# Performance work log

Hardware: AMD Instinct MI355X
Metric: run time of the kernel (lower is better)

Reference implementation:

```python
import jax, jax.numpy as jnp
import numpy as np

DIM = 2048
DIM_HEAD = 64
NUM_HEADS = 32
FFN_INNER = 4 * DIM  # 8192
SCALE = DIM_HEAD ** -0.5
LN_EPS = 1e-5


def setup_inputs() -> dict:
    key = jax.random.key(0)
    k1, k2, k3 = jax.random.split(key, 3)
    B, S = 2, 2048
    in_dim = FFN_INNER * 2 + DIM_HEAD * (NUM_HEADS + 2)  # 18560
    out_in = FFN_INNER + DIM  # 10240
    return {
        "x": jax.random.normal(k1, (B, S, DIM), jnp.float32),
        "W_in": jax.random.normal(k2, (DIM, in_dim), jnp.float32) * (DIM ** -0.5),
        "W_out": jax.random.normal(k3, (out_in, DIM), jnp.float32) * (out_in ** -0.5),
        "ln_gamma": jnp.ones((DIM,), jnp.float32),
        "ln_beta": jnp.zeros((DIM,), jnp.float32),
    }


def _rotary_pos(seq, d, dtype):
    inv_freq = 1.0 / (10000.0 ** (jnp.arange(0, d, 2, dtype=jnp.float32) / d))
    freqs = jnp.arange(seq, dtype=jnp.float32)[:, None] * inv_freq[None, :]  # [s, d/2]
    pos = jnp.concatenate([freqs, freqs], axis=-1)  # [s, d]
    return pos.astype(dtype)


def _rotate_half(t):
    d = t.shape[-1] // 2
    return jnp.concatenate([-t[..., d:], t[..., :d]], axis=-1)


def _apply_rotary(pos, t):
    return t * jnp.cos(pos) + _rotate_half(t) * jnp.sin(pos)


def reference(x, W_in, W_out, ln_gamma, ln_beta):
    B, S, D = x.shape
    # LayerNorm (residual uses the NORMED x, as in the source)
    mu = jnp.mean(x, axis=-1, keepdims=True)
    var = jnp.mean(jnp.square(x - mu), axis=-1, keepdims=True)
    xn = (x - mu) / jnp.sqrt(var + LN_EPS) * ln_gamma + ln_beta

    h = jnp.einsum('bsd,df->bsf', xn, W_in)  # fused input projection
    a = NUM_HEADS * DIM_HEAD  # attn inner dim
    q = h[..., :a]
    k = h[..., a:a + DIM_HEAD]                      # [b, s, d] shared (multi-query)
    v = h[..., a + DIM_HEAD:a + 2 * DIM_HEAD]       # [b, s, d]
    ffn_input = h[..., a + 2 * DIM_HEAD:a + 2 * DIM_HEAD + FFN_INNER]

    q = q.reshape(B, S, NUM_HEADS, DIM_HEAD).transpose(0, 2, 1, 3)  # b h s d

    pos = _rotary_pos(S, DIM_HEAD, x.dtype)
    q = _apply_rotary(pos, q)
    k = _apply_rotary(pos, k)
    q = q * SCALE

    sim = jnp.einsum('bhsd,bjd->bhsj', q, k)  # [b, h, s, s]
    causal = jnp.triu(jnp.ones((S, S), bool), 1)
    neg = jnp.finfo(sim.dtype).max
    sim = jnp.where(causal, -neg, sim)
    sim = sim - jax.lax.stop_gradient(jnp.max(sim, axis=-1, keepdims=True))
    attn = jax.nn.softmax(sim, axis=-1)

    attn_out = jnp.einsum('bhij,bjd->bhid', attn, v)  # b h s d
    attn_out = attn_out.transpose(0, 2, 1, 3).reshape(B, S, a)

    concat = jnp.concatenate([attn_out, ffn_input], axis=-1)  # [b, s, ffn+dim]
    out = jnp.einsum('bsf,fd->bsd', concat, W_out)
    return out + xn
```

## Files before the change

kernel.cpp:

```cpp
#include <hip/hip_runtime.h>
#include <cstdint>

#define NB     2
#define SEQ    2048
#define DIMN   2048
#define NROWS  (NB*SEQ)
#define NHEADS 32
#define DHEAD  64
#define FFN    8192
#define HC     10368
#define WINLD  18560
#define OI     10240

typedef __bf16 bf16_t;
typedef bf16_t bf16x8 __attribute__((ext_vector_type(8)));
typedef bf16_t bf16x4 __attribute__((ext_vector_type(4)));
typedef bf16_t bf16x2 __attribute__((ext_vector_type(2)));
typedef float  f32x4  __attribute__((ext_vector_type(4)));

typedef const uint32_t __attribute__((address_space(1)))* as1p;
typedef uint32_t __attribute__((address_space(3)))* as3p;

__device__ __forceinline__ void load_lds16(const void* g, void* l) {
  __builtin_amdgcn_global_load_lds(
      reinterpret_cast<as1p>(reinterpret_cast<uintptr_t>(g)),
      reinterpret_cast<as3p>(reinterpret_cast<uintptr_t>(l)),
      16, 0, 0);
}

__global__ __launch_bounds__(256) void ln_kernel(const float* __restrict__ x,
                                                 const float* __restrict__ gamma,
                                                 const float* __restrict__ beta,
                                                 bf16_t* __restrict__ xnb)
{
  const int row = blockIdx.x;
  const int t = threadIdx.x;
  const float4* xr = (const float4*)(x + (size_t)row * DIMN);
  float4 v0 = xr[t], v1 = xr[t + 256];
  float s  = v0.x+v0.y+v0.z+v0.w + v1.x+v1.y+v1.z+v1.w;
  float ss = v0.x*v0.x+v0.y*v0.y+v0.z*v0.z+v0.w*v0.w
           + v1.x*v1.x+v1.y*v1.y+v1.z*v1.z+v1.w*v1.w;
#pragma unroll
  for (int off = 32; off; off >>= 1) { s += __shfl_xor(s, off); ss += __shfl_xor(ss, off); }
  __shared__ float red[8];
  const int w = t >> 6;
  if ((t & 63) == 0) { red[w] = s; red[w + 4] = ss; }
  __syncthreads();
  s  = red[0]+red[1]+red[2]+red[3];
  ss = red[4]+red[5]+red[6]+red[7];
  const float mu   = s * (1.f/DIMN);
  const float var  = ss * (1.f/DIMN) - mu*mu;
  const float rstd = rsqrtf(var + 1e-5f);
  const float4* g4 = (const float4*)gamma;
  const float4* b4 = (const float4*)beta;
  float4 ga0 = g4[t], ga1 = g4[t+256], be0 = b4[t], be1 = b4[t+256];
  float4 y0, y1;
  y0.x = (v0.x-mu)*rstd*ga0.x + be0.x;  y0.y = (v0.y-mu)*rstd*ga0.y + be0.y;
  y0.z = (v0.z-mu)*rstd*ga0.z + be0.z;  y0.w = (v0.w-mu)*rstd*ga0.w + be0.w;
  y1.x = (v1.x-mu)*rstd*ga1.x + be1.x;  y1.y = (v1.y-mu)*rstd*ga1.y + be1.y;
  y1.z = (v1.z-mu)*rstd*ga1.z + be1.z;  y1.w = (v1.w-mu)*rstd*ga1.w + be1.w;
  bf16_t* xo = xnb + (size_t)row * DIMN;
  bf16x4 o0 = {(bf16_t)y0.x, (bf16_t)y0.y, (bf16_t)y0.z, (bf16_t)y0.w};
  bf16x4 o1 = {(bf16_t)y1.x, (bf16_t)y1.y, (bf16_t)y1.z, (bf16_t)y1.w};
  *(bf16x4*)(xo + t*4)        = o0;
  *(bf16x4*)(xo + (t+256)*4)  = o1;
}

__global__ __launch_bounds__(256) void tcast_kernel(const float* __restrict__ in, int ld_in,
                                                    bf16_t* __restrict__ out, int out_cols)
{
  __shared__ float tile[128][33];
  const int t = threadIdx.x;
  const int ic0 = blockIdx.x * 32;
  const int ir0 = blockIdx.y * 128;
#pragma unroll
  for (int k = 0; k < 16; k++) {
    const int idx = k*256 + t, row = idx >> 5, col = idx & 31;
    tile[row][col] = in[(size_t)(ir0 + row) * ld_in + ic0 + col];
  }
  __syncthreads();
#pragma unroll
  for (int k = 0; k < 8; k++) {
    const int idx = k*256 + t, r = idx >> 6, cp = idx & 63;
    bf16x2 v = {(bf16_t)tile[cp*2][r], (bf16_t)tile[cp*2 + 1][r]};
    *(bf16x2*)&out[(size_t)(ic0 + r) * out_cols + ir0 + cp*2] = v;
  }
}

#define BW_NONE ((void)0)
#define BW_VM   asm volatile("s_waitcnt vmcnt(%0)" :: "n"(VM))
#define BW_V0   asm volatile("s_waitcnt vmcnt(0)")

template<int BM, int BN, int KTOT, int OP>
__global__ __launch_bounds__(512, 2) void gemm8p(
    const bf16_t* __restrict__ A0p, const bf16_t* __restrict__ A1p,
    const bf16_t* __restrict__ Btp, const bf16_t* __restrict__ Res,
    bf16_t* __restrict__ Cb, float* __restrict__ Cf)
{
  constexpr int NT    = KTOT / 64;
  constexpr int NP    = NT / 2;
  constexpr int MR    = BM / 64;
  constexpr int NRr   = BN / 128;
  constexpr int ALPT  = BM / 128;
  constexpr int BLPT  = BN / 128;
  constexpr int VM    = ALPT + BLPT;
  constexpr int AHALF = (BM/2)*64;
  constexpr int BHALF = (BN/2)*64;
  constexpr int ABUF  = BM*64;
  constexpr int BUFSZ = ABUF + BN*64;
  constexpr int BLD   = OP ? OI : DIMN;
  constexpr int CPX   = OP ? 32 : 82;
  __shared__ __align__(16) bf16_t lds[2*BUFSZ];

  const int t = threadIdx.x;
  const int l = t & 63, w = t >> 6;
  const int wm2 = w >> 2, wn2 = w & 3;
  const int lr = l & 15, lq = l >> 4;

  const int id  = blockIdx.x;
  const int swz = (id & 7) * CPX + (id >> 3);
  int m0, n0;
  if (OP == 0) {
    m0 = (swz & 15) << 8;
    n0 = (swz >> 4) << 8;
    if (n0 > HC - 256) n0 = HC - 256;
  } else {
    m0 = (swz & 31) << 7;
    n0 = (swz >> 5) << 8;
  }

  const int rsw = (w << 3) | (l >> 3);
  const int csw = (((l & 7) ^ ((l >> 3) & 7)) << 3);
  const int axor[2] = { ((lq ^ (lr & 7)) << 3), (((4 + lq) ^ (lr & 7)) << 3) };
  const int arow = wm2*(BM/4) + lr;
  const int brow = wn2*(BN/8) + lr;

  auto stA = [&](int buf, int half, int kt) {
    const int k0 = kt * 64;
#pragma unroll
    for (int c = 0; c < ALPT; c++) {
      const int gr = m0 + half*(BM/2) + c*64 + rsw;
      const bf16_t* src;
      if (OP == 0 || k0 < DIMN) src = A0p + (size_t)gr * DIMN + k0 + csw;
      else                      src = A1p + (size_t)gr * HC + 2176 + (k0 - DIMN) + csw;
      load_lds16(src, lds + buf*BUFSZ + half*AHALF + c*4096 + (w << 9));
    }
  };
  auto stB = [&](int buf, int half, int kt) {
    const int k0 = kt * 64;
#pragma unroll
    for (int c = 0; c < BLPT; c++) {
      const int gr = n0 + half*(BN/2) + c*64 + rsw;
      load_lds16(Btp + (size_t)gr * BLD + k0 + csw,
                 lds + buf*BUFSZ + ABUF + half*BHALF + c*4096 + (w << 9));
    }
  };

  f32x4 acc[2][2][MR][NRr];
  const f32x4 z4 = {0.f,0.f,0.f,0.f};
#pragma unroll
  for (int qm = 0; qm < 2; qm++)
#pragma unroll
    for (int qn = 0; qn < 2; qn++)
#pragma unroll
      for (int i = 0; i < MR; i++)
#pragma unroll
        for (int j = 0; j < NRr; j++) acc[qm][qn][i][j] = z4;

  stA(0,0,0); stA(0,1,0); stB(0,0,0); stB(0,1,0);
  stA(1,0,1); stB(1,0,1);
  BW_VM;
  __builtin_amdgcn_sched_barrier(0);
  __builtin_amdgcn_s_barrier();
  __builtin_amdgcn_sched_barrier(0);

#define PHASE(BUF, QM, QN, STAGE, BWAIT)                                      \
  {                                                                           \
    bf16x8 af[MR][2], bfr[NRr][2];                                            \
    _Pragma("unroll")                                                         \
    for (int i_ = 0; i_ < MR; i_++)                                           \
      _Pragma("unroll")                                                       \
      for (int kk_ = 0; kk_ < 2; kk_++)                                       \
        af[i_][kk_] = *(const bf16x8*)&lds[(BUF)*BUFSZ + (QM)*AHALF           \
                        + (arow + i_*16)*64 + axor[kk_]];                     \
    _Pragma("unroll")                                                         \
    for (int j_ = 0; j_ < NRr; j_++)                                          \
      _Pragma("unroll")                                                       \
      for (int kk_ = 0; kk_ < 2; kk_++)                                       \
        bfr[j_][kk_] = *(const bf16x8*)&lds[(BUF)*BUFSZ + ABUF + (QN)*BHALF   \
                        + (brow + j_*16)*64 + axor[kk_]];                     \
    STAGE;                                                                    \
    __builtin_amdgcn_s_barrier();                                             \
    __builtin_amdgcn_sched_barrier(0);                                        \
    __builtin_amdgcn_s_setprio(1);                                            \
    _Pragma("unroll")                                                         \
    for (int i_ = 0; i_ < MR; i_++)                                           \
      _Pragma("unroll")                                                       \
      for (int j_ = 0; j_ < NRr; j_++)                                        \
        _Pragma("unroll")                                                     \
        for (int kk_ = 0; kk_ < 2; kk_++)                                     \
          acc[QM][QN][i_][j_] = __builtin_amdgcn_mfma_f32_16x16x32_bf16(      \
              af[i_][kk_], bfr[j_][kk_], acc[QM][QN][i_][j_], 0, 0, 0);       \
    __builtin_amdgcn_s_setprio(0);                                            \
    BWAIT;                                                                    \
    __builtin_amdgcn_s_barrier();                                             \
    __builtin_amdgcn_sched_barrier(0);                                        \
  }

  for (int it = 0; it < NP-1; it++) {
    const int e = 2*it, o = e+1;
    PHASE(0,0,0, stA(1,1,o),   BW_NONE)
    PHASE(0,0,1, stB(1,1,o),   BW_NONE)
    PHASE(0,1,0, stA(0,0,e+2), BW_NONE)
    PHASE(0,1,1, stB(0,0,e+2), BW_VM)
    PHASE(1,0,0, stA(0,1,e+2), BW_NONE)
    PHASE(1,0,1, stB(0,1,e+2), BW_NONE)
    PHASE(1,1,0, stA(1,0,o+2), BW_NONE)
    PHASE(1,1,1, stB(1,0,o+2), BW_VM)
  }
  {
    const int o = NT-1;
    PHASE(0,0,0, stA(1,1,o), BW_NONE)
    PHASE(0,0,1, stB(1,1,o), BW_NONE)
    PHASE(0,1,0, BW_NONE,    BW_NONE)
    PHASE(0,1,1, BW_NONE,    BW_V0)
    PHASE(1,0,0, BW_NONE,    BW_NONE)
    PHASE(1,0,1, BW_NONE,    BW_NONE)
    PHASE(1,1,0, BW_NONE,    BW_NONE)
    PHASE(1,1,1, BW_NONE,    BW_NONE)
  }
#undef PHASE

#pragma unroll
  for (int qm = 0; qm < 2; qm++)
#pragma unroll
    for (int qn = 0; qn < 2; qn++)
#pragma unroll
      for (int i = 0; i < MR; i++)
#pragma unroll
        for (int j = 0; j < NRr; j++) {
          const int row = m0 + qm*(BM/2) + wm2*(BM/4) + i*16 + lq*4;
          const int col = n0 + qn*(BN/2) + wn2*(BN/8) + j*16 + lr;
#pragma unroll
          for (int r = 0; r < 4; r++) {
            if (OP == 0) {
              Cb[(size_t)(row + r) * HC + col] = (bf16_t)acc[qm][qn][i][j][r];
            } else {
              const size_t idx = (size_t)(row + r) * DIMN + col;
              Cf[idx] = acc[qm][qn][i][j][r] + (float)Res[idx];
            }
          }
        }
}

__global__ __launch_bounds__(256) void rope_kernel(bf16_t* __restrict__ H, bf16_t* __restrict__ Vt)
{
  const int row = blockIdx.x;
  const int s = row & (SEQ - 1);
  const int b = row >> 11;
  bf16_t* hr = H + (size_t)row * HC;
  const int t = threadIdx.x;
  for (int task = t; task < 1056; task += 256) {
    const int hd = task >> 5, j = task & 31;
    const int base = (hd < 32) ? hd*64 : 2048;
    const float inv = exp2f(-(float)j * 0.41524101186092437f);
    const float ang = (float)s * inv;
    float sn, cs;
    sincosf(ang, &sn, &cs);
    const float x1 = (float)hr[base + j], x2 = (float)hr[base + j + 32];
    const float sc = (hd < 32) ? 0.125f : 1.0f;
    hr[base + j]      = (bf16_t)((x1*cs - x2*sn) * sc);
    hr[base + j + 32] = (bf16_t)((x2*cs + x1*sn) * sc);
  }
  for (int d = t; d < 64; d += 256)
    Vt[(size_t)(b*64 + d) * SEQ + s] = hr[2112 + d];
}

template<int NTMAX, bool MASK>
__device__ __forceinline__ void attn_tile_body(
    const bf16_t* __restrict__ Qs, const bf16_t* __restrict__ Ks,
    const bf16_t* __restrict__ Vts, bf16_t* __restrict__ Ps,
    f32x4 (&accO)[4], float (&m_run)[4], float (&l_run)[4],
    int w, int lr, int lq, int q0, int j0)
{
  const f32x4 z4 = {0.f,0.f,0.f,0.f};
  f32x4 accS[NTMAX];
#pragma unroll
  for (int i = 0; i < NTMAX; i++) accS[i] = z4;
  bf16x8 aq[2];
#pragma unroll
  for (int kt = 0; kt < 2; kt++)
    aq[kt] = *(const bf16x8*)&Qs[(w*16 + lr)*72 + kt*32 + lq*8];
#pragma unroll
  for (int nt = 0; nt < NTMAX; nt++)
#pragma unroll
    for (int kt = 0; kt < 2; kt++) {
      bf16x8 bk = *(const bf16x8*)&Ks[(nt*16 + lr)*72 + kt*32 + lq*8];
      accS[nt] = __builtin_amdgcn_mfma_f32_16x16x32_bf16(aq[kt], bk, accS[nt], 0, 0, 0);
    }
  if (MASK) {
    const int rg0 = q0 + w*16 + lq*4;
#pragma unroll
    for (int nt = 0; nt < NTMAX; nt++) {
      const int cg = j0 + nt*16 + lr;
#pragma unroll
      for (int r = 0; r < 4; r++)
        if (cg > rg0 + r) accS[nt][r] = -3.0e38f;
    }
  }
  float al[4];
#pragma unroll
  for (int r = 0; r < 4; r++) {
    float m = accS[0][r];
#pragma unroll
    for (int nt = 1; nt < NTMAX; nt++) m = fmaxf(m, accS[nt][r]);
    m = fmaxf(m, __shfl_xor(m, 1)); m = fmaxf(m, __shfl_xor(m, 2));
    m = fmaxf(m, __shfl_xor(m, 4)); m = fmaxf(m, __shfl_xor(m, 8));
    const float nm = fmaxf(m_run[r], m);
    al[r] = __expf(m_run[r] - nm);
    m_run[r] = nm;
  }
#pragma unroll
  for (int nt = 0; nt < NTMAX; nt++)
#pragma unroll
    for (int r = 0; r < 4; r++)
      accS[nt][r] = __expf(accS[nt][r] - m_run[r]);
#pragma unroll
  for (int r = 0; r < 4; r++) {
    float sum = 0.f;
#pragma unroll
    for (int nt = 0; nt < NTMAX; nt++) sum += accS[nt][r];
    sum += __shfl_xor(sum, 1); sum += __shfl_xor(sum, 2);
    sum += __shfl_xor(sum, 4); sum += __shfl_xor(sum, 8);
    l_run[r] = l_run[r]*al[r] + sum;
  }
#pragma unroll
  for (int nt = 0; nt < 4; nt++)
#pragma unroll
    for (int r = 0; r < 4; r++) accO[nt][r] *= al[r];
#pragma unroll
  for (int nt = 0; nt < NTMAX; nt++)
#pragma unroll
    for (int r = 0; r < 4; r++)
      Ps[(w*16 + lq*4 + r)*136 + nt*16 + lr] = (bf16_t)accS[nt][r];
  __syncthreads();
#pragma unroll
  for (int kt = 0; kt < NTMAX/2; kt++) {
    bf16x8 ap = *(const bf16x8*)&Ps[(w*16 + lr)*136 + kt*32 + lq*8];
#pragma unroll
    for (int nt = 0; nt < 4; nt++) {
      bf16x8 bv = *(const bf16x8*)&Vts[(nt*16 + lr)*136 + kt*32 + lq*8];
      accO[nt] = __builtin_amdgcn_mfma_f32_16x16x32_bf16(ap, bv, accO[nt], 0, 0, 0);
    }
  }
}

__global__ __launch_bounds__(256, 2) void attn_kernel(const bf16_t* __restrict__ H,
                                                      const bf16_t* __restrict__ Vt,
                                                      bf16_t* __restrict__ AttnOut)
{
  __shared__ __align__(16) bf16_t Qs[64*72];
  __shared__ __align__(16) bf16_t Ks[128*72];
  __shared__ __align__(16) bf16_t Vts[64*136];
  __shared__ __align__(16) bf16_t Ps[64*136];
  const int t = threadIdx.x, l = t & 63, w = t >> 6, lr = l & 15, lq = l >> 4;
  const int qb = blockIdx.x, head = blockIdx.y, b = blockIdx.z;
  const int q0 = qb * 64;
  const size_t hbase = (size_t)(b * SEQ) * HC;

#pragma unroll
  for (int i = 0; i < 2; i++) {
    const int id = t + i*256, row = id >> 3, ch = (id & 7) << 3;
    bf16x8 v = *(const bf16x8*)&H[hbase + (size_t)(q0 + row) * HC + head*64 + ch];
    *(bf16x8*)&Qs[row*72 + ch] = v;
  }
  f32x4 accO[4];
  const f32x4 z4 = {0.f,0.f,0.f,0.f};
#pragma unroll
  for (int i = 0; i < 4; i++) accO[i] = z4;
  float m_run[4], l_run[4];
#pragma unroll
  for (int r = 0; r < 4; r++) { m_run[r] = -3.0e38f; l_run[r] = 0.f; }
  const int ntiles = (qb >> 1) + 1;
  __syncthreads();

  for (int tile = 0; tile < ntiles; tile++) {
    const int j0 = tile * 128;
#pragma unroll
    for (int i = 0; i < 4; i++) {
      const int id = t + i*256, row = id >> 3, ch = (id & 7) << 3;
      bf16x8 v = *(const bf16x8*)&H[hbase + (size_t)(j0 + row) * HC + 2048 + ch];
      *(bf16x8*)&Ks[row*72 + ch] = v;
    }
#pragma unroll
    for (int i = 0; i < 4; i++) {
      const int id = t + i*256, row = id >> 4, ch = (id & 15) << 3;
      bf16x8 v = *(const bf16x8*)&Vt[(size_t)(b*64 + row) * SEQ + j0 + ch];
      *(bf16x8*)&Vts[row*136 + ch] = v;
    }
    __syncthreads();
    if (tile < ntiles - 1)
      attn_tile_body<8,false>(Qs, Ks, Vts, Ps, accO, m_run, l_run, w, lr, lq, q0, j0);
    else if ((qb & 1) == 0)
      attn_tile_body<4,true >(Qs, Ks, Vts, Ps, accO, m_run, l_run, w, lr, lq, q0, j0);
    else
      attn_tile_body<8,true >(Qs, Ks, Vts, Ps, accO, m_run, l_run, w, lr, lq, q0, j0);
    __syncthreads();
  }
  float inv_l[4];
#pragma unroll
  for (int r = 0; r < 4; r++) inv_l[r] = 1.f / l_run[r];
#pragma unroll
  for (int nt = 0; nt < 4; nt++)
#pragma unroll
    for (int r = 0; r < 4; r++)
      AttnOut[(size_t)(b*SEQ + q0 + w*16 + lq*4 + r) * DIMN + head*64 + nt*16 + lr]
          = (bf16_t)(accO[nt][r] * inv_l[r]);
}

extern "C" void kernel_launch(void* const* d_in, const int* in_sizes, int n_in,
                              void* d_out, int out_size, void* d_ws, size_t ws_size,
                              hipStream_t stream)
{
  const float* x     = (const float*)d_in[0];
  const float* W_in  = (const float*)d_in[1];
  const float* W_out = (const float*)d_in[2];
  const float* gamma = (const float*)d_in[3];
  const float* beta  = (const float*)d_in[4];
  float* out = (float*)d_out;

  char* ws = (char*)d_ws;
  bf16_t* xnb   = (bf16_t*)(ws);
  bf16_t* h     = (bf16_t*)(ws + 16777216);
  bf16_t* WinT  = (bf16_t*)(ws + 101711872);
  bf16_t* WoutT = (bf16_t*)(ws + 144179200);
  bf16_t* Vt    = (bf16_t*)(ws + 186122240);
  bf16_t* attn  = (bf16_t*)(ws + 186646528);

  ln_kernel<<<NROWS, 256, 0, stream>>>(x, gamma, beta, xnb);
  tcast_kernel<<<dim3(HC/32, DIMN/128), 256, 0, stream>>>(W_in, WINLD, WinT, DIMN);
  tcast_kernel<<<dim3(DIMN/32, OI/128), 256, 0, stream>>>(W_out, DIMN, WoutT, OI);
  gemm8p<256,256,DIMN,0><<<656, 512, 0, stream>>>(xnb, nullptr, WinT, nullptr, h, nullptr);
  rope_kernel<<<NROWS, 256, 0, stream>>>(h, Vt);
  attn_kernel<<<dim3(SEQ/64, NHEADS, NB), 256, 0, stream>>>(h, Vt, attn);
  gemm8p<128,256,OI,1><<<256, 512, 0, stream>>>(attn, h, WoutT, xnb, nullptr, out);
}
```

Before: 872.8 us.

## Restructure attention with 128-row tiles, causal load balancing, and K/V double buffering

The attention kernel now uses 512-thread blocks over 128-row query tiles. Each block processes a pair of query blocks (pid and 15-pid) so causal work is balanced across blocks. The next K/V tile is prefetched into registers and written into a second LDS buffer while QK and softmax run on the current one. MFMA sections get raised wave priority. The larger LDS footprint may reduce occupancy to one block per CU.

```diff
diff --git a/kernel.cpp b/kernel.cpp
--- a/kernel.cpp
+++ b/kernel.cpp
@@ -276,32 +276,34 @@
     Vt[(size_t)(b*64 + d) * SEQ + s] = hr[2112 + d];
 }
 
-template<int NTMAX, bool MASK>
-__device__ __forceinline__ void attn_tile_body(
+template<bool MASK>
+__device__ __forceinline__ void attn_qk_sm(
     const bf16_t* __restrict__ Qs, const bf16_t* __restrict__ Ks,
-    const bf16_t* __restrict__ Vts, bf16_t* __restrict__ Ps,
+    bf16_t* __restrict__ Ps,
     f32x4 (&accO)[4], float (&m_run)[4], float (&l_run)[4],
     int w, int lr, int lq, int q0, int j0)
 {
   const f32x4 z4 = {0.f,0.f,0.f,0.f};
-  f32x4 accS[NTMAX];
-#pragma unroll
-  for (int i = 0; i < NTMAX; i++) accS[i] = z4;
+  f32x4 accS[8];
+#pragma unroll
+  for (int i = 0; i < 8; i++) accS[i] = z4;
   bf16x8 aq[2];
 #pragma unroll
   for (int kt = 0; kt < 2; kt++)
     aq[kt] = *(const bf16x8*)&Qs[(w*16 + lr)*72 + kt*32 + lq*8];
-#pragma unroll
-  for (int nt = 0; nt < NTMAX; nt++)
+  __builtin_amdgcn_s_setprio(1);
+#pragma unroll
+  for (int nt = 0; nt < 8; nt++)
 #pragma unroll
     for (int kt = 0; kt < 2; kt++) {
       bf16x8 bk = *(const bf16x8*)&Ks[(nt*16 + lr)*72 + kt*32 + lq*8];
       accS[nt] = __builtin_amdgcn_mfma_f32_16x16x32_bf16(aq[kt], bk, accS[nt], 0, 0, 0);
     }
+  __builtin_amdgcn_s_setprio(0);
   if (MASK) {
     const int rg0 = q0 + w*16 + lq*4;
 #pragma unroll
-    for (int nt = 0; nt < NTMAX; nt++) {
+    for (int nt = 0; nt < 8; nt++) {
       const int cg = j0 + nt*16 + lr;
 #pragma unroll
       for (int r = 0; r < 4; r++)
@@ -313,7 +315,7 @@
   for (int r = 0; r < 4; r++) {
     float m = accS[0][r];
 #pragma unroll
-    for (int nt = 1; nt < NTMAX; nt++) m = fmaxf(m, accS[nt][r]);
+    for (int nt = 1; nt < 8; nt++) m = fmaxf(m, accS[nt][r]);
     m = fmaxf(m, __shfl_xor(m, 1)); m = fmaxf(m, __shfl_xor(m, 2));
     m = fmaxf(m, __shfl_xor(m, 4)); m = fmaxf(m, __shfl_xor(m, 8));
     const float nm = fmaxf(m_run[r], m);
@@ -321,7 +323,7 @@
     m_run[r] = nm;
   }
 #pragma unroll
-  for (int nt = 0; nt < NTMAX; nt++)
+  for (int nt = 0; nt < 8; nt++)
 #pragma unroll
     for (int r = 0; r < 4; r++)
       accS[nt][r] = __expf(accS[nt][r] - m_run[r]);
@@ -329,7 +331,7 @@
   for (int r = 0; r < 4; r++) {
     float sum = 0.f;
 #pragma unroll
-    for (int nt = 0; nt < NTMAX; nt++) sum += accS[nt][r];
+    for (int nt = 0; nt < 8; nt++) sum += accS[nt][r];
     sum += __shfl_xor(sum, 1); sum += __shfl_xor(sum, 2);
     sum += __shfl_xor(sum, 4); sum += __shfl_xor(sum, 8);
     l_run[r] = l_run[r]*al[r] + sum;
@@ -339,13 +341,19 @@
 #pragma unroll
     for (int r = 0; r < 4; r++) accO[nt][r] *= al[r];
 #pragma unroll
-  for (int nt = 0; nt < NTMAX; nt++)
+  for (int nt = 0; nt < 8; nt++)
 #pragma unroll
     for (int r = 0; r < 4; r++)
       Ps[(w*16 + lq*4 + r)*136 + nt*16 + lr] = (bf16_t)accS[nt][r];
-  __syncthreads();
-#pragma unroll
-  for (int kt = 0; kt < NTMAX/2; kt++) {
+}
+
+__device__ __forceinline__ void attn_pv(
+    const bf16_t* __restrict__ Ps, const bf16_t* __restrict__ Vts,
+    f32x4 (&accO)[4], int w, int lr, int lq)
+{
+  __builtin_amdgcn_s_setprio(1);
+#pragma unroll
+  for (int kt = 0; kt < 4; kt++) {
     bf16x8 ap = *(const bf16x8*)&Ps[(w*16 + lr)*136 + kt*32 + lq*8];
 #pragma unroll
     for (int nt = 0; nt < 4; nt++) {
@@ -353,69 +361,88 @@
       accO[nt] = __builtin_amdgcn_mfma_f32_16x16x32_bf16(ap, bv, accO[nt], 0, 0, 0);
     }
   }
-}
-
-__global__ __launch_bounds__(256, 2) void attn_kernel(const bf16_t* __restrict__ H,
+  __builtin_amdgcn_s_setprio(0);
+}
+
+__global__ __launch_bounds__(512, 2) void attn_kernel(const bf16_t* __restrict__ H,
                                                       const bf16_t* __restrict__ Vt,
                                                       bf16_t* __restrict__ AttnOut)
 {
-  __shared__ __align__(16) bf16_t Qs[64*72];
-  __shared__ __align__(16) bf16_t Ks[128*72];
-  __shared__ __align__(16) bf16_t Vts[64*136];
-  __shared__ __align__(16) bf16_t Ps[64*136];
+  __shared__ __align__(16) bf16_t Qs[128*72];
+  __shared__ __align__(16) bf16_t Ks[2][128*72];
+  __shared__ __align__(16) bf16_t Vts[2][64*136];
+  __shared__ __align__(16) bf16_t Ps[128*136];
   const int t = threadIdx.x, l = t & 63, w = t >> 6, lr = l & 15, lq = l >> 4;
-  const int qb = blockIdx.x, head = blockIdx.y, b = blockIdx.z;
-  const int q0 = qb * 64;
+  const int pid = blockIdx.x, head = blockIdx.y, b = blockIdx.z;
   const size_t hbase = (size_t)(b * SEQ) * HC;
-
-#pragma unroll
-  for (int i = 0; i < 2; i++) {
-    const int id = t + i*256, row = id >> 3, ch = (id & 7) << 3;
-    bf16x8 v = *(const bf16x8*)&H[hbase + (size_t)(q0 + row) * HC + head*64 + ch];
-    *(bf16x8*)&Qs[row*72 + ch] = v;
-  }
-  f32x4 accO[4];
-  const f32x4 z4 = {0.f,0.f,0.f,0.f};
-#pragma unroll
-  for (int i = 0; i < 4; i++) accO[i] = z4;
-  float m_run[4], l_run[4];
-#pragma unroll
-  for (int r = 0; r < 4; r++) { m_run[r] = -3.0e38f; l_run[r] = 0.f; }
-  const int ntiles = (qb >> 1) + 1;
-  __syncthreads();
-
-  for (int tile = 0; tile < ntiles; tile++) {
-    const int j0 = tile * 128;
-#pragma unroll
-    for (int i = 0; i < 4; i++) {
-      const int id = t + i*256, row = id >> 3, ch = (id & 7) << 3;
-      bf16x8 v = *(const bf16x8*)&H[hbase + (size_t)(j0 + row) * HC + 2048 + ch];
-      *(bf16x8*)&Ks[row*72 + ch] = v;
-    }
-#pragma unroll
-    for (int i = 0; i < 4; i++) {
-      const int id = t + i*256, row = id >> 4, ch = (id & 15) << 3;
-      bf16x8 v = *(const bf16x8*)&Vt[(size_t)(b*64 + row) * SEQ + j0 + ch];
-      *(bf16x8*)&Vts[row*136 + ch] = v;
-    }
+  const int kch = (t & 7) << 3, vch = (t & 15) << 3;
+
+  for (int half = 0; half < 2; half++) {
+    const int qb = half ? (15 - pid) : pid;
+    const int q0 = qb << 7;
+    const int ntiles = qb + 1;
+    bf16x8 kr[2], vr[2], qr[2];
+#pragma unroll
+    for (int i = 0; i < 2; i++) {
+      const int id = t + i*512;
+      qr[i] = *(const bf16x8*)&H[hbase + (size_t)(q0 + (id>>3)) * HC + head*64 + ((id&7)<<3)];
+      kr[i] = *(const bf16x8*)&H[hbase + (size_t)(id>>3) * HC + 2048 + kch];
+      vr[i] = *(const bf16x8*)&Vt[(size_t)(b*64 + (id>>4)) * SEQ + vch];
+    }
+#pragma unroll
+    for (int i = 0; i < 2; i++) {
+      const int id = t + i*512;
+      *(bf16x8*)&Qs[(id>>3)*72 + ((id&7)<<3)] = qr[i];
+      *(bf16x8*)&Ks[0][(id>>3)*72 + kch] = kr[i];
+      *(bf16x8*)&Vts[0][(id>>4)*136 + vch] = vr[i];
+    }
+    f32x4 accO[4];
+    const f32x4 z4 = {0.f,0.f,0.f,0.f};
+#pragma unroll
+    for (int i = 0; i < 4; i++) accO[i] = z4;
+    float m_run[4], l_run[4];
+#pragma unroll
+    for (int r = 0; r < 4; r++) { m_run[r] = -3.0e38f; l_run[r] = 0.f; }
     __syncthreads();
-    if (tile < ntiles - 1)
-      attn_tile_body<8,false>(Qs, Ks, Vts, Ps, accO, m_run, l_run, w, lr, lq, q0, j0);
-    else if ((qb & 1) == 0)
-      attn_tile_body<4,true >(Qs, Ks, Vts, Ps, accO, m_run, l_run, w, lr, lq, q0, j0);
-    else
-      attn_tile_body<8,true >(Qs, Ks, Vts, Ps, accO, m_run, l_run, w, lr, lq, q0, j0);
-    __syncthreads();
-  }
-  float inv_l[4];
-#pragma unroll
-  for (int r = 0; r < 4; r++) inv_l[r] = 1.f / l_run[r];
-#pragma unroll
-  for (int nt = 0; nt < 4; nt++)
-#pragma unroll
-    for (int r = 0; r < 4; r++)
-      AttnOut[(size_t)(b*SEQ + q0 + w*16 + lq*4 + r) * DIMN + head*64 + nt*16 + lr]
-          = (bf16_t)(accO[nt][r] * inv_l[r]);
+
+    for (int tile = 0; tile < ntiles; tile++) {
+      const int cur = tile & 1;
+      const bool last = (tile == ntiles - 1);
+      if (!last) {
+        const int j1 = (tile + 1) << 7;
+#pragma unroll
+        for (int i = 0; i < 2; i++) {
+          const int id = t + i*512;
+          kr[i] = *(const bf16x8*)&H[hbase + (size_t)(j1 + (id>>3)) * HC + 2048 + kch];
+          vr[i] = *(const bf16x8*)&Vt[(size_t)(b*64 + (id>>4)) * SEQ + j1 + vch];
+        }
+      }
+      if (last)
+        attn_qk_sm<true >(Qs, Ks[cur], Ps, accO, m_run, l_run, w, lr, lq, q0, tile<<7);
+      else
+        attn_qk_sm<false>(Qs, Ks[cur], Ps, accO, m_run, l_run, w, lr, lq, q0, tile<<7);
+      if (!last) {
+#pragma unroll
+        for (int i = 0; i < 2; i++) {
+          const int id = t + i*512;
+          *(bf16x8*)&Ks[cur^1][(id>>3)*72 + kch] = kr[i];
+          *(bf16x8*)&Vts[cur^1][(id>>4)*136 + vch] = vr[i];
+        }
+      }
+      __syncthreads();
+      attn_pv(Ps, Vts[cur], accO, w, lr, lq);
+      __syncthreads();
+    }
+    float inv_l[4];
+#pragma unroll
+    for (int r = 0; r < 4; r++) inv_l[r] = 1.f / l_run[r];
+#pragma unroll
+    for (int nt = 0; nt < 4; nt++)
+#pragma unroll
+      for (int r = 0; r < 4; r++)
+        AttnOut[(size_t)(b*SEQ + q0 + w*16 + lq*4 + r) * DIMN + head*64 + nt*16 + lr]
+            = (bf16_t)(accO[nt][r] * inv_l[r]);
+  }
 }
 
 extern "C" void kernel_launch(void* const* d_in, const int* in_sizes, int n_in,
@@ -442,6 +469,6 @@
   tcast_kernel<<<dim3(DIMN/32, OI/128), 256, 0, stream>>>(W_out, DIMN, WoutT, OI);
   gemm8p<256,256,DIMN,0><<<656, 512, 0, stream>>>(xnb, nullptr, WinT, nullptr, h, nullptr);
   rope_kernel<<<NROWS, 256, 0, stream>>>(h, Vt);
-  attn_kernel<<<dim3(SEQ/64, NHEADS, NB), 256, 0, stream>>>(h, Vt, attn);
+  attn_kernel<<<dim3(8, NHEADS, NB), 512, 0, stream>>>(h, Vt, attn);
   gemm8p<128,256,OI,1><<<256, 512, 0, stream>>>(attn, h, WoutT, xnb, nullptr, out);
 }
```

Result: faster. 797.3 us (-8.7%).
